# Performance work log

Measured on AMD Instinct MI355X. Metric: run time of the kernel, lower is better.

## Reference

```python
import jax, jax.numpy as jnp
import numpy as np

DIM = 512
HEADS = 8
NUM_KEYS = 256
TOPK = 16
B, T = 2, 2048
EPS = 1e-5  # BatchNorm1d default eps


def setup_inputs() -> dict:
    key = jax.random.key(0)
    ks = jax.random.split(key, 4)
    d_head = DIM // HEADS
    return {
        "x": jax.random.normal(ks[0], (B, T, DIM), jnp.float32),
        # nn.Linear(dim, dim, bias=False): weight (out, in), y = x @ W^T
        "Wq": jax.random.normal(ks[1], (DIM, DIM), jnp.float32) / np.sqrt(DIM),
        "gamma": jnp.ones((DIM,), jnp.float32),   # BatchNorm affine weight
        "beta": jnp.zeros((DIM,), jnp.float32),   # BatchNorm affine bias
        "keys": jax.random.normal(ks[2], (HEADS, NUM_KEYS, 2, d_head // 2), jnp.float32),
        "values": jax.random.normal(ks[3], (NUM_KEYS ** 2, DIM), jnp.float32),
    }


def reference(x, Wq, gamma, beta, keys, values):
    b, t, e = x.shape
    h, nk, k = HEADS, NUM_KEYS, TOPK
    # dropout layers are identity (p=0.0)
    q = jnp.einsum('bte,fe->btf', x, Wq)
    # MergeDims(BatchNorm1d) in training mode: batch stats over (b*t), biased var
    flat = q.reshape(-1, e)
    mean = flat.mean(axis=0)
    var = jnp.var(flat, axis=0)
    qn = ((flat - mean) * jax.lax.rsqrt(var + EPS) * gamma + beta).reshape(b, t, e)
    # chunk(2, dim=-1) then stack -> (2, b, t, h, d_head//2)
    qs = jnp.stack(jnp.split(qn, 2, axis=-1)).reshape(2, b, t, h, -1)
    dots = jnp.einsum('pbthd,hnpd->bthpn', qs, keys)  # (b,t,h,2,num_keys)
    scores, indices = jax.lax.top_k(dots, k)          # (b,t,h,2,k), sorted desc
    # faithful to source: chunk(2, dim=2) splits the HEAD axis
    h2 = h // 2
    s_a, s_b = scores[:, :, :h2], scores[:, :, h2:]    # (b,t,h/2,2,k)
    i_a, i_b = indices[:, :, :h2], indices[:, :, h2:]
    all_scores = (s_a[..., :, None] + s_b[..., None, :]).reshape(b, t, h, k * k)
    all_indices = (i_a[..., :, None] * nk + i_b[..., None, :]).reshape(b, t, h, k * k)
    final_scores, final_idx = jax.lax.top_k(all_scores, k)         # (b,t,h,k)
    value_indices = jnp.take_along_axis(all_indices, final_idx, axis=-1)
    attn = jax.nn.softmax(final_scores, axis=-1)
    vi = value_indices.reshape(-1, k * h)   # (b*t, k*h)
    w = attn.reshape(-1, k * h)
    # EmbeddingBag(mode='sum') with per_sample_weights
    out = jnp.einsum('nk,nkd->nd', w, values[vi])
    return out.reshape(b, t, e)
```

## Files before the change

kernel.cpp:

```cpp
#include <hip/hip_runtime.h>

#define NTOK 4096
#define EPS 1e-5f

__global__ void k_zero(float* __restrict__ stats) {
    int t = blockIdx.x * blockDim.x + threadIdx.x;
    if (t < 1024) stats[t] = 0.0f;
}

__global__ __launch_bounds__(256) void k_gemm(const float* __restrict__ A,
                                              const float* __restrict__ B,
                                              float* __restrict__ C,
                                              float* __restrict__ stats) {
    __shared__ float As[32][68];
    __shared__ float Bs[32][68];
    const int tid  = threadIdx.x;
    const int row0 = blockIdx.x * 64;
    const int col0 = blockIdx.y * 64;
    const int lr = tid >> 3;
    const int lc = (tid & 7) << 2;
    const int tx = tid & 15;
    const int ty = tid >> 4;
    float acc[4][4] = {};
    for (int kc = 0; kc < 512; kc += 32) {
        float4 a0 = *(const float4*)(A + (row0 + lr)      * 512 + kc + lc);
        float4 a1 = *(const float4*)(A + (row0 + lr + 32) * 512 + kc + lc);
        float4 b0 = *(const float4*)(B + (col0 + lr)      * 512 + kc + lc);
        float4 b1 = *(const float4*)(B + (col0 + lr + 32) * 512 + kc + lc);
        __syncthreads();
        As[lc + 0][lr] = a0.x; As[lc + 1][lr] = a0.y; As[lc + 2][lr] = a0.z; As[lc + 3][lr] = a0.w;
        As[lc + 0][lr + 32] = a1.x; As[lc + 1][lr + 32] = a1.y; As[lc + 2][lr + 32] = a1.z; As[lc + 3][lr + 32] = a1.w;
        Bs[lc + 0][lr] = b0.x; Bs[lc + 1][lr] = b0.y; Bs[lc + 2][lr] = b0.z; Bs[lc + 3][lr] = b0.w;
        Bs[lc + 0][lr + 32] = b1.x; Bs[lc + 1][lr + 32] = b1.y; Bs[lc + 2][lr + 32] = b1.z; Bs[lc + 3][lr + 32] = b1.w;
        __syncthreads();
        #pragma unroll
        for (int k = 0; k < 32; ++k) {
            const float4 av = *(const float4*)&As[k][ty << 2];
            const float4 bv = *(const float4*)&Bs[k][tx << 2];
            const float a[4] = {av.x, av.y, av.z, av.w};
            const float b[4] = {bv.x, bv.y, bv.z, bv.w};
            #pragma unroll
            for (int i = 0; i < 4; ++i)
                #pragma unroll
                for (int j = 0; j < 4; ++j)
                    acc[i][j] += a[i] * b[j];
        }
    }
    #pragma unroll
    for (int i = 0; i < 4; ++i) {
        float4 v = make_float4(acc[i][0], acc[i][1], acc[i][2], acc[i][3]);
        *(float4*)(C + (row0 + ty * 4 + i) * 512 + col0 + (tx << 2)) = v;
    }
    __syncthreads();
    float* redS = &As[0][0];
    float* redQ = &Bs[0][0];
    #pragma unroll
    for (int j = 0; j < 4; ++j) {
        const float s = acc[0][j] + acc[1][j] + acc[2][j] + acc[3][j];
        const float qq = acc[0][j] * acc[0][j] + acc[1][j] * acc[1][j]
                       + acc[2][j] * acc[2][j] + acc[3][j] * acc[3][j];
        redS[ty * 64 + tx * 4 + j] = s;
        redQ[ty * 64 + tx * 4 + j] = qq;
    }
    __syncthreads();
    if (tid < 64) {
        float a = 0.0f, b = 0.0f;
        #pragma unroll
        for (int t = 0; t < 16; ++t) {
            a += redS[t * 64 + tid];
            b += redQ[t * 64 + tid];
        }
        atomicAdd(&stats[col0 + tid], a);
        atomicAdd(&stats[512 + col0 + tid], b);
    }
}

__global__ void k_finalize(const float* __restrict__ stats, float* __restrict__ mr) {
    const int f = threadIdx.x;
    const float mean = stats[f] * (1.0f / 4096.0f);
    const float var  = stats[512 + f] * (1.0f / 4096.0f) - mean * mean;
    mr[f]       = mean;
    mr[512 + f] = rsqrtf(var + EPS);
}

__device__ __forceinline__ unsigned int fmono(float x) {
    const unsigned int u = __float_as_uint(x);
    return (u & 0x80000000u) ? ~u : (u | 0x80000000u);
}

__device__ __forceinline__ unsigned int wave_max_u32(unsigned int m) {
    unsigned int t;
    t = (unsigned int)__builtin_amdgcn_update_dpp(0, (int)m, 0x121, 0xF, 0xF, true); m = t > m ? t : m;
    t = (unsigned int)__builtin_amdgcn_update_dpp(0, (int)m, 0x122, 0xF, 0xF, true); m = t > m ? t : m;
    t = (unsigned int)__builtin_amdgcn_update_dpp(0, (int)m, 0x124, 0xF, 0xF, true); m = t > m ? t : m;
    t = (unsigned int)__builtin_amdgcn_update_dpp(0, (int)m, 0x128, 0xF, 0xF, true); m = t > m ? t : m;
    t = (unsigned int)__builtin_amdgcn_update_dpp(0, (int)m, 0x142, 0xF, 0xF, true); m = t > m ? t : m;
    t = (unsigned int)__builtin_amdgcn_update_dpp(0, (int)m, 0x143, 0xF, 0xF, true); m = t > m ? t : m;
    return (unsigned int)__builtin_amdgcn_readlane((int)m, 63);
}

__global__ __launch_bounds__(256, 4) void k_pkm(
    const float* __restrict__ q,
    const float* __restrict__ mr,
    const float* __restrict__ gamma,
    const float* __restrict__ beta,
    const float* __restrict__ keys,
    const float* __restrict__ values,
    float* __restrict__ out)
{
    __shared__ float qn[512];
    __shared__ float sTopS[16][16];
    __shared__ int   sTopI[16][16];
    __shared__ float wW[128];
    __shared__ int   wI[128];

    const int tok  = blockIdx.x;
    const int tid  = threadIdx.x;
    const int lane = tid & 63;
    const int wave = tid >> 6;

    {
        const float v0 = q[tok * 512 + tid];
        const float v1 = q[tok * 512 + 256 + tid];
        qn[tid]       = (v0 - mr[tid]) * mr[512 + tid] * gamma[tid] + beta[tid];
        qn[tid + 256] = (v1 - mr[tid + 256]) * mr[512 + tid + 256] * gamma[tid + 256] + beta[tid + 256];
    }
    __syncthreads();

    unsigned int cand[4][4];
    #pragma unroll
    for (int s4 = 0; s4 < 4; ++s4) {
        const int s = wave * 4 + s4;
        const int h = s >> 1;
        const int p = s & 1;
        const float4* qp4 = (const float4*)&qn[p * 256 + h * 32];
        #pragma unroll
        for (int j = 0; j < 4; ++j) {
            const int n = lane + 64 * j;
            const float4* kp4 = (const float4*)(keys + ((h * 256 + n) * 2 + p) * 32);
            float dot = 0.0f;
            #pragma unroll
            for (int d4 = 0; d4 < 8; ++d4) {
                const float4 kv = kp4[d4];
                const float4 qf = qp4[d4];
                dot += qf.x * kv.x + qf.y * kv.y + qf.z * kv.z + qf.w * kv.w;
            }
            cand[s4][j] = (fmono(dot) & 0xFFFFFF00u) | (unsigned int)(255 - n);
        }
    }

    unsigned int mywin1 = 0;
    #pragma unroll
    for (int it = 0; it < 16; ++it) {
        #pragma unroll
        for (int s4 = 0; s4 < 4; ++s4) {
            unsigned int lm = cand[s4][0];
            #pragma unroll
            for (int j = 1; j < 4; ++j) lm = (cand[s4][j] > lm) ? cand[s4][j] : lm;
            const unsigned int win = wave_max_u32(lm);
            if (lane == s4 * 16 + it) mywin1 = win;
            #pragma unroll
            for (int j = 0; j < 4; ++j) if (cand[s4][j] == win) cand[s4][j] = 0u;
        }
    }
    {
        const int s = wave * 4 + (lane >> 4);
        const int h = s >> 1;
        const int p = s & 1;
        const int n = 255 - (int)(mywin1 & 0xFFu);
        const float4* qp4 = (const float4*)&qn[p * 256 + h * 32];
        const float4* kp4 = (const float4*)(keys + ((h * 256 + n) * 2 + p) * 32);
        float dot = 0.0f;
        #pragma unroll
        for (int d4 = 0; d4 < 8; ++d4) {
            const float4 kv = kp4[d4];
            const float4 qf = qp4[d4];
            dot += qf.x * kv.x + qf.y * kv.y + qf.z * kv.z + qf.w * kv.w;
        }
        sTopS[s][lane & 15] = dot;
        sTopI[s][lane & 15] = n;
    }
    __syncthreads();

    unsigned int c2[2][4];
    #pragma unroll
    for (int r2 = 0; r2 < 2; ++r2) {
        const int hh = wave * 2 + r2;
        const int ha = hh >> 1;
        const int p  = hh & 1;
        const int sa = ha * 2 + p;
        const int sb = (ha + 4) * 2 + p;
        const float sAv = sTopS[sa][lane >> 2];
        #pragma unroll
        for (int j = 0; j < 4; ++j) {
            const int c = lane * 4 + j;
            const float sc = sAv + sTopS[sb][c & 15];
            c2[r2][j] = (fmono(sc) & 0xFFFFFF00u) | (unsigned int)(255 - c);
        }
    }
    unsigned int mywin2 = 0;
    #pragma unroll
    for (int it = 0; it < 16; ++it) {
        #pragma unroll
        for (int r2 = 0; r2 < 2; ++r2) {
            unsigned int lm = c2[r2][0];
            #pragma unroll
            for (int j = 1; j < 4; ++j) lm = (c2[r2][j] > lm) ? c2[r2][j] : lm;
            const unsigned int win = wave_max_u32(lm);
            if (lane == r2 * 16 + it) mywin2 = win;
            #pragma unroll
            for (int j = 0; j < 4; ++j) if (c2[r2][j] == win) c2[r2][j] = 0u;
        }
    }
    if (lane < 32) {
        const int r2 = lane >> 4;
        const int hh = wave * 2 + r2;
        const int ha = hh >> 1;
        const int p  = hh & 1;
        const int sa = ha * 2 + p;
        const int sb = (ha + 4) * 2 + p;
        const int c  = 255 - (int)(mywin2 & 0xFFu);
        const float sc = sTopS[sa][c >> 4] + sTopS[sb][c & 15];
        const float mx = __shfl(sc, lane & 48);
        const float e  = __expf(sc - mx);
        float ssum = e;
        #pragma unroll
        for (int off = 1; off < 16; off <<= 1) ssum += __shfl_xor(ssum, off);
        wW[hh * 16 + (lane & 15)] = e / ssum;
        wI[hh * 16 + (lane & 15)] = sTopI[sa][c >> 4] * 256 + sTopI[sb][c & 15];
    }
    __syncthreads();

    float2 acc = make_float2(0.0f, 0.0f);
    const float2* vb = (const float2*)values;
    #pragma unroll 8
    for (int k = 0; k < 128; ++k) {
        const float w   = wW[k];
        const int   idx = wI[k];
        const float2 v  = vb[idx * 256 + tid];
        acc.x += w * v.x;
        acc.y += w * v.y;
    }
    *(float2*)(out + tok * 512 + tid * 2) = acc;
}

extern "C" void kernel_launch(void* const* d_in, const int* in_sizes, int n_in,
                              void* d_out, int out_size, void* d_ws, size_t ws_size,
                              hipStream_t stream) {
    const float* x      = (const float*)d_in[0];
    const float* Wq     = (const float*)d_in[1];
    const float* gamma  = (const float*)d_in[2];
    const float* beta   = (const float*)d_in[3];
    const float* keys   = (const float*)d_in[4];
    const float* values = (const float*)d_in[5];
    float* out = (float*)d_out;

    float* q     = (float*)d_ws;
    float* stats = q + NTOK * 512;
    float* mr    = stats + 1024;

    k_zero<<<1, 1024, 0, stream>>>(stats);
    dim3 g1(NTOK / 64, 512 / 64);
    k_gemm<<<g1, 256, 0, stream>>>(x, Wq, q, stats);
    k_finalize<<<1, 512, 0, stream>>>(stats, mr);
    k_pkm<<<NTOK, 256, 0, stream>>>(q, mr, gamma, beta, keys, values, out);
}
```

Before: 538.6 us.

## Split PKM kernel into separate top-k selection and value-gather kernels

The fused per-token kernel is split in two. The first does normalization, key scoring and top-k selection, and writes softmax weights and value indices into the token's now-unused slot of the q workspace. The second kernel reads those and performs the weighted embedding-bag gather. The split lets each kernel target higher occupancy (launch bounds raised to 8) and separates the compute-bound selection from the memory-bound gather. It also caches the query slice in registers during the dot products. The cost is an extra launch and a small global round trip. Overwriting q in place is safe only because each block touches just its own token's row.

```diff
diff --git a/kernel.cpp b/kernel.cpp
--- a/kernel.cpp
+++ b/kernel.cpp
@@ -99,20 +99,16 @@
     return (unsigned int)__builtin_amdgcn_readlane((int)m, 63);
 }
 
-__global__ __launch_bounds__(256, 4) void k_pkm(
-    const float* __restrict__ q,
+__global__ __launch_bounds__(256, 8) void k_sel(
+    float* __restrict__ q,
     const float* __restrict__ mr,
     const float* __restrict__ gamma,
     const float* __restrict__ beta,
-    const float* __restrict__ keys,
-    const float* __restrict__ values,
-    float* __restrict__ out)
+    const float* __restrict__ keys)
 {
     __shared__ float qn[512];
     __shared__ float sTopS[16][16];
     __shared__ int   sTopI[16][16];
-    __shared__ float wW[128];
-    __shared__ int   wI[128];
 
     const int tok  = blockIdx.x;
     const int tid  = threadIdx.x;
@@ -133,7 +129,9 @@
         const int s = wave * 4 + s4;
         const int h = s >> 1;
         const int p = s & 1;
-        const float4* qp4 = (const float4*)&qn[p * 256 + h * 32];
+        float4 qf[8];
+        #pragma unroll
+        for (int d4 = 0; d4 < 8; ++d4) qf[d4] = ((const float4*)&qn[p * 256 + h * 32])[d4];
         #pragma unroll
         for (int j = 0; j < 4; ++j) {
             const int n = lane + 64 * j;
@@ -142,8 +140,7 @@
             #pragma unroll
             for (int d4 = 0; d4 < 8; ++d4) {
                 const float4 kv = kp4[d4];
-                const float4 qf = qp4[d4];
-                dot += qf.x * kv.x + qf.y * kv.y + qf.z * kv.z + qf.w * kv.w;
+                dot += qf[d4].x * kv.x + qf[d4].y * kv.y + qf[d4].z * kv.z + qf[d4].w * kv.w;
             }
             cand[s4][j] = (fmono(dot) & 0xFFFFFF00u) | (unsigned int)(255 - n);
         }
@@ -226,20 +223,33 @@
         float ssum = e;
         #pragma unroll
         for (int off = 1; off < 16; off <<= 1) ssum += __shfl_xor(ssum, off);
-        wW[hh * 16 + (lane & 15)] = e / ssum;
-        wI[hh * 16 + (lane & 15)] = sTopI[sa][c >> 4] * 256 + sTopI[sb][c & 15];
-    }
-    __syncthreads();
-
+        q[tok * 512 + hh * 16 + (lane & 15)] = e / ssum;
+        ((int*)q)[tok * 512 + 128 + hh * 16 + (lane & 15)] =
+            sTopI[sa][c >> 4] * 256 + sTopI[sb][c & 15];
+    }
+}
+
+__global__ __launch_bounds__(256, 8) void k_gather(
+    const float* __restrict__ q,
+    const float* __restrict__ values,
+    float* __restrict__ out)
+{
+    __shared__ float w[128];
+    __shared__ int   idx[128];
+    const int tok = blockIdx.x;
+    const int tid = threadIdx.x;
+    if (tid < 128) {
+        w[tid]   = q[tok * 512 + tid];
+        idx[tid] = ((const int*)q)[tok * 512 + 128 + tid];
+    }
+    __syncthreads();
     float2 acc = make_float2(0.0f, 0.0f);
     const float2* vb = (const float2*)values;
     #pragma unroll 8
     for (int k = 0; k < 128; ++k) {
-        const float w   = wW[k];
-        const int   idx = wI[k];
-        const float2 v  = vb[idx * 256 + tid];
-        acc.x += w * v.x;
-        acc.y += w * v.y;
+        const float2 v = vb[idx[k] * 256 + tid];
+        acc.x += w[k] * v.x;
+        acc.y += w[k] * v.y;
     }
     *(float2*)(out + tok * 512 + tid * 2) = acc;
 }
@@ -263,5 +273,6 @@
     dim3 g1(NTOK / 64, 512 / 64);
     k_gemm<<<g1, 256, 0, stream>>>(x, Wq, q, stats);
     k_finalize<<<1, 512, 0, stream>>>(stats, mr);
-    k_pkm<<<NTOK, 256, 0, stream>>>(q, mr, gamma, beta, keys, values, out);
-}
+    k_sel<<<NTOK, 256, 0, stream>>>(q, mr, gamma, beta, keys);
+    k_gather<<<NTOK, 256, 0, stream>>>(q, values, out);
+}
```

New measurement: 613.0 us. 13.8% more time.
